# Performance work log

Measured on AMD Instinct MI355X. Metric: run time of the kernel, lower is better.

## Reference

```python
import jax, jax.numpy as jnp
import numpy as np

N, E, D = 50000, 500000, 128   # nodes, edges, input feature dim
H, F = 4, 32                    # num_heads, features_per_head (H*F == MLP output 128)


def _layer_norm(x, scale, bias, eps=1e-6):
    mu = jnp.mean(x, axis=-1, keepdims=True)
    var = jnp.var(x, axis=-1, keepdims=True)
    return (x - mu) * jax.lax.rsqrt(var + eps) * scale + bias


def setup_inputs() -> dict:
    key = jax.random.key(0)
    ks = jax.random.split(key, 6)
    s = lambda fan_in: 1.0 / np.sqrt(fan_in)
    return {
        "nodes": jax.random.normal(ks[0], (N, D), jnp.float32),
        "W1": jax.random.normal(ks[1], (D, 128), jnp.float32) * s(D),
        "b1": jnp.zeros((128,), jnp.float32),
        "ln1_scale": jnp.ones((128,), jnp.float32),
        "ln1_bias": jnp.zeros((128,), jnp.float32),
        "W2": jax.random.normal(ks[2], (128, H * F), jnp.float32) * s(128),
        "b2": jnp.zeros((H * F,), jnp.float32),
        "ln2_scale": jnp.ones((H * F,), jnp.float32),
        "ln2_bias": jnp.zeros((H * F,), jnp.float32),
        "senders": jax.random.randint(ks[3], (E,), 0, N, dtype=jnp.int32),
        "receivers": jax.random.randint(ks[4], (E,), 0, N, dtype=jnp.int32),
    }


def reference(nodes, W1, b1, ln1_scale, ln1_bias, W2, b2, ln2_scale, ln2_bias,
              senders, receivers):
    # attention_query MLP (MLPTorso: Dense -> LayerNorm -> relu, activate_final=True)
    h = jnp.maximum(_layer_norm(nodes @ W1 + b1, ln1_scale, ln1_bias), 0.0)
    h = jnp.maximum(_layer_norm(h @ W2 + b2, ln2_scale, ln2_bias), 0.0)
    q = h.reshape(N, H, F)                       # [N, H, F]

    # gather per-edge sender/receiver projections (same math as per-edge MLP)
    sent = q[senders]                            # [E, H, F]
    recv = q[receivers]                          # [E, H, F]

    # per-edge, per-head attention logits
    logits = jnp.einsum('ehf,ehf->eh', sent, recv) / jnp.sqrt(jnp.float32(F))

    # segment softmax over incoming edges of each receiver node (jraph semantics)
    seg_max = jax.ops.segment_max(logits, receivers, num_segments=N)
    seg_max = jnp.where(jnp.isfinite(seg_max), seg_max, 0.0)  # empty segments
    unnorm = jnp.exp(logits - seg_max[receivers])
    denom = jax.ops.segment_sum(unnorm, receivers, num_segments=N)
    weights = unnorm / denom[receivers]          # [E, H]

    # weighted messages, scatter-sum to receiver nodes
    messages = sent * weights[..., None]         # [E, H, F]
    agg = jax.ops.segment_sum(messages, receivers, num_segments=N)  # [N, H, F]

    # node update: activation then average over heads (avg_multi_head=True)
    out = jnp.maximum(agg, 0.0)
    return jnp.mean(out, axis=1)                 # [N, F]
```

## Files before the change

kernel.cpp:

```cpp
#include <hip/hip_runtime.h>

constexpr int D  = 128;
constexpr int NH = 4;
constexpr int NF = 32;

typedef __attribute__((ext_vector_type(8))) short bfrag;
typedef __attribute__((ext_vector_type(4))) float ffrag;

__device__ __forceinline__ unsigned short bf16h(float x) {
    unsigned u = __float_as_uint(x);
    u += 0x7fffu + ((u >> 16) & 1u);
    return (unsigned short)(u >> 16);
}
__device__ __forceinline__ float bf16tof(unsigned short h) {
    return __uint_as_float(((unsigned)h) << 16);
}

__global__ __launch_bounds__(256) void zero_cnt_kernel(int* __restrict__ p, int n)
{
    const int i4 = (blockIdx.x * blockDim.x + threadIdx.x) * 4;
    if (i4 + 3 < n) {
        *(int4*)&p[i4] = {0, 0, 0, 0};
    } else if (i4 < n) {
        for (int i = i4; i < n; ++i) p[i] = 0;
    }
}

__global__ __launch_bounds__(256) void wsplit_kernel(
    const float* __restrict__ W1, const float* __restrict__ W2,
    unsigned short* __restrict__ wt)
{
    __shared__ float T[32][33];
    const int L  = blockIdx.x >> 4;
    const int t  = blockIdx.x & 15;
    const int tr = t >> 2, tc = t & 3;
    const float* W = L ? W2 : W1;
    unsigned short* Hp = wt + (size_t)L * 32768;
    unsigned short* Lp = Hp + 16384;
    const int tx = threadIdx.x & 31, ty = threadIdx.x >> 5;
    #pragma unroll
    for (int i = 0; i < 4; ++i)
        T[ty + 8*i][tx] = W[(size_t)(tr*32 + ty + 8*i) * 128 + tc*32 + tx];
    __syncthreads();
    #pragma unroll
    for (int i = 0; i < 4; ++i) {
        const int c = tc*32 + ty + 8*i;
        const int k = tr*32 + tx;
        const float v = T[tx][ty + 8*i];
        const unsigned short hh = bf16h(v);
        const unsigned short ll = bf16h(v - bf16tof(hh));
        Hp[c*128 + k] = hh;
        Lp[c*128 + k] = ll;
    }
}

__global__ __launch_bounds__(256, 2) void mlp_mfma_kernel(
    const float* __restrict__ X,
    const unsigned short* __restrict__ WT,
    const float* __restrict__ b1, const float* __restrict__ g1, const float* __restrict__ be1,
    const float* __restrict__ b2, const float* __restrict__ g2, const float* __restrict__ be2,
    unsigned short* __restrict__ Q, int N)
{
    constexpr int P = 136;
    __shared__ unsigned short Xh[64 * P];
    __shared__ unsigned short Xl[64 * P];
    __shared__ unsigned short Wh[64 * P];
    __shared__ unsigned short Wl[64 * P];

    const int tid  = threadIdx.x;
    const int lane = tid & 63;
    const int wave = tid >> 6;
    const int n0   = blockIdx.x * 64;
    const int lc   = lane & 15;
    const int lg   = lane >> 4;

    #pragma unroll
    for (int j = 0; j < 8; ++j) {
        const int idx = tid + 256 * j;
        const int row = idx >> 5;
        const int c4  = (idx & 31) * 4;
        float4 v = {0, 0, 0, 0};
        if (n0 + row < N) v = *(const float4*)&X[(size_t)(n0 + row) * 128 + c4];
        const unsigned short h0 = bf16h(v.x), h1 = bf16h(v.y),
                             h2 = bf16h(v.z), h3 = bf16h(v.w);
        const unsigned short q0 = bf16h(v.x - bf16tof(h0)),
                             q1 = bf16h(v.y - bf16tof(h1)),
                             q2 = bf16h(v.z - bf16tof(h2)),
                             q3 = bf16h(v.w - bf16tof(h3));
        uint2 ph, pl;
        ph.x = (unsigned)h0 | ((unsigned)h1 << 16);
        ph.y = (unsigned)h2 | ((unsigned)h3 << 16);
        pl.x = (unsigned)q0 | ((unsigned)q1 << 16);
        pl.y = (unsigned)q2 | ((unsigned)q3 << 16);
        *(uint2*)&Xh[row * P + c4] = ph;
        *(uint2*)&Xl[row * P + c4] = pl;
    }

    auto stageW = [&](const unsigned short* Hg, const unsigned short* Lg, int half) {
        #pragma unroll
        for (int j = 0; j < 4; ++j) {
            const int u = tid + 256 * j;
            const int c = u >> 4;
            const int t = (u & 15) * 8;
            *(uint4*)&Wh[c * P + t] = *(const uint4*)&Hg[(size_t)(half*64 + c) * 128 + t];
            *(uint4*)&Wl[c * P + t] = *(const uint4*)&Lg[(size_t)(half*64 + c) * 128 + t];
        }
    };

    bfrag ah[4], al[4];
    auto loadA = [&]() {
        const int arow = wave * 16 + lc;
        #pragma unroll
        for (int ks = 0; ks < 4; ++ks) {
            ah[ks] = *(const bfrag*)&Xh[arow * P + ks * 32 + lg * 8];
            al[ks] = *(const bfrag*)&Xl[arow * P + ks * 32 + lg * 8];
        }
    };

    ffrag acc[8];
    auto gemmHalf = [&](int half) {
        #pragma unroll
        for (int ct = 0; ct < 4; ++ct) {
            const int crow = ct * 16 + lc;
            bfrag bh[4], bl[4];
            #pragma unroll
            for (int ks = 0; ks < 4; ++ks) {
                bh[ks] = *(const bfrag*)&Wh[crow * P + ks * 32 + lg * 8];
                bl[ks] = *(const bfrag*)&Wl[crow * P + ks * 32 + lg * 8];
            }
            ffrag a = acc[half * 4 + ct];
            #pragma unroll
            for (int ks = 0; ks < 4; ++ks) {
                a = __builtin_amdgcn_mfma_f32_16x16x32_bf16(ah[ks], bh[ks], a, 0, 0, 0);
                a = __builtin_amdgcn_mfma_f32_16x16x32_bf16(ah[ks], bl[ks], a, 0, 0, 0);
                a = __builtin_amdgcn_mfma_f32_16x16x32_bf16(al[ks], bh[ks], a, 0, 0, 0);
            }
            acc[half * 4 + ct] = a;
        }
    };

    const unsigned short* W1h = WT;
    const unsigned short* W1l = WT + 16384;
    const unsigned short* W2h = WT + 32768;
    const unsigned short* W2l = WT + 49152;

    #pragma unroll
    for (int i = 0; i < 8; ++i) acc[i] = (ffrag){0.f, 0.f, 0.f, 0.f};

    stageW(W1h, W1l, 0);
    __syncthreads();
    loadA();
    gemmHalf(0);
    __syncthreads();
    stageW(W1h, W1l, 1);
    __syncthreads();
    gemmHalf(1);

    {
        float bb[8], gg[8], tt[8];
        #pragma unroll
        for (int ct = 0; ct < 8; ++ct) {
            const int col = ct * 16 + lc;
            bb[ct] = b1[col]; gg[ct] = g1[col]; tt[ct] = be1[col];
        }
        #pragma unroll
        for (int j = 0; j < 4; ++j) {
            float t[8], s = 0.f, ss = 0.f;
            #pragma unroll
            for (int ct = 0; ct < 8; ++ct) {
                t[ct] = acc[ct][j] + bb[ct];
                s += t[ct]; ss += t[ct] * t[ct];
            }
            #pragma unroll
            for (int off = 1; off <= 8; off <<= 1) {
                s  += __shfl_xor(s,  off, 16);
                ss += __shfl_xor(ss, off, 16);
            }
            const float mu   = s * (1.f / 128.f);
            const float var  = fmaxf(ss * (1.f / 128.f) - mu * mu, 0.f);
            const float rstd = rsqrtf(var + 1e-6f);
            const int rl = wave * 16 + lg * 4 + j;
            #pragma unroll
            for (int ct = 0; ct < 8; ++ct) {
                const float o = fmaxf((t[ct] - mu) * rstd * gg[ct] + tt[ct], 0.f);
                const unsigned short hh = bf16h(o);
                const unsigned short ll = bf16h(o - bf16tof(hh));
                Xh[rl * P + ct * 16 + lc] = hh;
                Xl[rl * P + ct * 16 + lc] = ll;
            }
        }
    }

    #pragma unroll
    for (int i = 0; i < 8; ++i) acc[i] = (ffrag){0.f, 0.f, 0.f, 0.f};

    __syncthreads();
    stageW(W2h, W2l, 0);
    __syncthreads();
    loadA();
    gemmHalf(0);
    __syncthreads();
    stageW(W2h, W2l, 1);
    __syncthreads();
    gemmHalf(1);

    {
        float bb[8], gg[8], tt[8];
        #pragma unroll
        for (int ct = 0; ct < 8; ++ct) {
            const int col = ct * 16 + lc;
            bb[ct] = b2[col]; gg[ct] = g2[col]; tt[ct] = be2[col];
        }
        #pragma unroll
        for (int j = 0; j < 4; ++j) {
            float t[8], s = 0.f, ss = 0.f;
            #pragma unroll
            for (int ct = 0; ct < 8; ++ct) {
                t[ct] = acc[ct][j] + bb[ct];
                s += t[ct]; ss += t[ct] * t[ct];
            }
            #pragma unroll
            for (int off = 1; off <= 8; off <<= 1) {
                s  += __shfl_xor(s,  off, 16);
                ss += __shfl_xor(ss, off, 16);
            }
            const float mu   = s * (1.f / 128.f);
            const float var  = fmaxf(ss * (1.f / 128.f) - mu * mu, 0.f);
            const float rstd = rsqrtf(var + 1e-6f);
            const int grow = n0 + wave * 16 + lg * 4 + j;
            if (grow < N) {
                #pragma unroll
                for (int ct = 0; ct < 8; ++ct) {
                    const float o = fmaxf((t[ct] - mu) * rstd * gg[ct] + tt[ct], 0.f);
                    Q[(size_t)grow * 128 + ct * 16 + lc] = bf16h(o);
                }
            }
        }
    }
}

__global__ __launch_bounds__(256) void hist_kernel(
    const int* __restrict__ recv, int* __restrict__ cnt, int E)
{
    int i = blockIdx.x * blockDim.x + threadIdx.x;
    if (i < E) atomicAdd(&cnt[recv[i]], 1);
}

__global__ __launch_bounds__(256) void scan_blocks_kernel(
    const int* __restrict__ cnt, int* __restrict__ rowptr,
    int* __restrict__ bsum, int N)
{
    __shared__ int lds[256];
    const int tid = threadIdx.x;
    const int base = blockIdx.x * 1024 + tid * 4;
    int v0 = (base + 0 < N) ? cnt[base + 0] : 0;
    int v1 = (base + 1 < N) ? cnt[base + 1] : 0;
    int v2 = (base + 2 < N) ? cnt[base + 2] : 0;
    int v3 = (base + 3 < N) ? cnt[base + 3] : 0;
    const int tsum = v0 + v1 + v2 + v3;
    lds[tid] = tsum;
    __syncthreads();
    for (int off = 1; off < 256; off <<= 1) {
        int t = (tid >= off) ? lds[tid - off] : 0;
        __syncthreads();
        lds[tid] += t;
        __syncthreads();
    }
    int run = lds[tid] - tsum;
    if (base + 0 < N) rowptr[base + 0] = run;
    run += v0;
    if (base + 1 < N) rowptr[base + 1] = run;
    run += v1;
    if (base + 2 < N) rowptr[base + 2] = run;
    run += v2;
    if (base + 3 < N) rowptr[base + 3] = run;
    if (tid == 255) bsum[blockIdx.x] = lds[255];
}

__global__ __launch_bounds__(256) void scan_top_kernel(int* bsum, int nb)
{
    __shared__ int lds[256];
    const int tid = threadIdx.x;
    int v = (tid < nb) ? bsum[tid] : 0;
    lds[tid] = v;
    __syncthreads();
    for (int off = 1; off < 256; off <<= 1) {
        int t = (tid >= off) ? lds[tid - off] : 0;
        __syncthreads();
        lds[tid] += t;
        __syncthreads();
    }
    if (tid < nb) bsum[tid] = lds[tid] - v;
}

__global__ __launch_bounds__(256) void scan_add_kernel(
    int* __restrict__ rowptr, int* __restrict__ cursor,
    const int* __restrict__ bsum, int N, int E)
{
    int i = blockIdx.x * blockDim.x + threadIdx.x;
    if (i < N) {
        int v = rowptr[i] + bsum[i >> 10];
        rowptr[i] = v;
        cursor[i] = v;
    }
    if (i == 0) rowptr[N] = E;
}

__global__ __launch_bounds__(256) void fill_kernel(
    const int* __restrict__ senders, const int* __restrict__ receivers,
    int* __restrict__ cursor, int* __restrict__ ssend, int E)
{
    int e = blockIdx.x * blockDim.x + threadIdx.x;
    if (e < E) {
        int r = receivers[e];
        int pos = atomicAdd(&cursor[r], 1);
        ssend[pos] = senders[e];
    }
}

__global__ __launch_bounds__(256) void node_attn_kernel(
    const unsigned short* __restrict__ q, const int* __restrict__ rowptr,
    const int* __restrict__ ssend, float* __restrict__ out, int N)
{
    const int lane = threadIdx.x & 63;
    const int hl   = lane & 31;
    const int half = lane >> 5;
    const int wid  = (blockIdx.x * blockDim.x + threadIdx.x) >> 6;
    const int nw   = (gridDim.x * blockDim.x) >> 6;

    for (int n = wid; n < N; n += nw) {
        const uint2 braw = *(const uint2*)&q[(size_t)n * D + hl * 4];
        const float b0 = __uint_as_float(braw.x << 16);
        const float b1 = __uint_as_float(braw.x & 0xffff0000u);
        const float b2 = __uint_as_float(braw.y << 16);
        const float b3 = __uint_as_float(braw.y & 0xffff0000u);

        const int beg = rowptr[n], end = rowptr[n + 1];
        float m = -1e30f, l = 0.f;
        float c0 = 0.f, c1 = 0.f, c2 = 0.f, c3 = 0.f;

        int j = beg + half;
        uint2 raw = {0u, 0u};
        if (j < end)
            raw = *(const uint2*)&q[(size_t)ssend[j] * D + hl * 4];
        for (; j < end; j += 2) {
            const uint2 cur = raw;
            if (j + 2 < end)
                raw = *(const uint2*)&q[(size_t)ssend[j + 2] * D + hl * 4];
            const float a0 = __uint_as_float(cur.x << 16);
            const float a1 = __uint_as_float(cur.x & 0xffff0000u);
            const float a2 = __uint_as_float(cur.y << 16);
            const float a3 = __uint_as_float(cur.y & 0xffff0000u);
            float p = a0 * b0 + a1 * b1 + a2 * b2 + a3 * b3;
            p += __shfl_xor(p, 1);
            p += __shfl_xor(p, 2);
            p += __shfl_xor(p, 4);
            const float logit = p * 0.17677669529663687f;
            const float nm = fmaxf(m, logit);
            const float sc = __expf(m - nm);
            const float u  = __expf(logit - nm);
            l  = l * sc + u;
            c0 = c0 * sc + u * a0;
            c1 = c1 * sc + u * a1;
            c2 = c2 * sc + u * a2;
            c3 = c3 * sc + u * a3;
            m = nm;
        }

        const float om  = __shfl_xor(m, 32);
        const float ol  = __shfl_xor(l, 32);
        const float oc0 = __shfl_xor(c0, 32);
        const float oc1 = __shfl_xor(c1, 32);
        const float oc2 = __shfl_xor(c2, 32);
        const float oc3 = __shfl_xor(c3, 32);
        const float nm = fmaxf(m, om);
        const float s0 = __expf(m - nm), s1 = __expf(om - nm);
        const float lt = l * s0 + ol * s1;
        const float inv = (lt > 0.f) ? (1.f / lt) : 0.f;
        float r0 = fmaxf((c0 * s0 + oc0 * s1) * inv, 0.f);
        float r1 = fmaxf((c1 * s0 + oc1 * s1) * inv, 0.f);
        float r2 = fmaxf((c2 * s0 + oc2 * s1) * inv, 0.f);
        float r3 = fmaxf((c3 * s0 + oc3 * s1) * inv, 0.f);

        r0 += __shfl_xor(r0, 8);  r0 += __shfl_xor(r0, 16);
        r1 += __shfl_xor(r1, 8);  r1 += __shfl_xor(r1, 16);
        r2 += __shfl_xor(r2, 8);  r2 += __shfl_xor(r2, 16);
        r3 += __shfl_xor(r3, 8);  r3 += __shfl_xor(r3, 16);
        if (lane < 8) {
            float4 o = {0.25f * r0, 0.25f * r1, 0.25f * r2, 0.25f * r3};
            *(float4*)&out[(size_t)n * NF + lane * 4] = o;
        }
    }
}

extern "C" void kernel_launch(void* const* d_in, const int* in_sizes, int n_in,
                              void* d_out, int out_size, void* d_ws, size_t ws_size,
                              hipStream_t stream)
{
    const float* nodes = (const float*)d_in[0];
    const float* W1    = (const float*)d_in[1];
    const float* b1    = (const float*)d_in[2];
    const float* g1    = (const float*)d_in[3];
    const float* be1   = (const float*)d_in[4];
    const float* W2    = (const float*)d_in[5];
    const float* b2    = (const float*)d_in[6];
    const float* g2    = (const float*)d_in[7];
    const float* be2   = (const float*)d_in[8];
    const int* senders   = (const int*)d_in[9];
    const int* receivers = (const int*)d_in[10];

    const int N = in_sizes[0] / D;
    const int E = in_sizes[9];
    float* out = (float*)d_out;

    char* ws = (char*)d_ws;
    unsigned short* qb = (unsigned short*)ws; ws += (size_t)N * D * 2;
    unsigned short* wt = (unsigned short*)ws; ws += 4 * 128 * 128 * 2;
    int* cnt      = (int*)ws;    ws += (size_t)N * 4;
    int* rowptr   = (int*)ws;    ws += (size_t)(N + 2) * 4;
    int* cursor   = (int*)ws;    ws += (size_t)N * 4;
    int* bsum     = (int*)ws;    ws += 256 * 4;
    int* ssend    = (int*)ws;    ws += (size_t)E * 4;

    zero_cnt_kernel<<<(N / 4 + 255) / 256, 256, 0, stream>>>(cnt, N);

    wsplit_kernel<<<32, 256, 0, stream>>>(W1, W2, wt);
    const int gblk = (N + 63) / 64;
    mlp_mfma_kernel<<<gblk, 256, 0, stream>>>(nodes, wt, b1, g1, be1,
                                              b2, g2, be2, qb, N);

    const int nb = (N + 1023) / 1024;
    hist_kernel<<<(E + 255) / 256, 256, 0, stream>>>(receivers, cnt, E);
    scan_blocks_kernel<<<nb, 256, 0, stream>>>(cnt, rowptr, bsum, N);
    scan_top_kernel<<<1, 256, 0, stream>>>(bsum, nb);
    scan_add_kernel<<<(N + 255) / 256, 256, 0, stream>>>(rowptr, cursor, bsum, N, E);
    fill_kernel<<<(E + 255) / 256, 256, 0, stream>>>(senders, receivers, cursor, ssend, E);

    node_attn_kernel<<<(N + 3) / 4, 256, 0, stream>>>(qb, rowptr, ssend, out, N);
}
```

Measured before the change: 134.4 us.

## Pre-swizzle weights into MFMA fragment order and drop shared-memory staging in MLP

The weight-split kernel now writes W1/W2 hi/lo bf16 parts directly in per-lane MFMA fragment order. The MLP kernel then loads B fragments straight from global memory (L2-resident) instead of staging them through shared memory with block barriers. Each wave processes its own 16 rows independently, converting X in registers and round-tripping the hidden layer through a small per-wave LDS buffer. This removes __syncthreads and cuts LDS use so the launch bound can rise to 4 blocks per CU, at the cost of repeated global/L2 weight fetches per wave.

```diff
diff --git a/kernel.cpp b/kernel.cpp
--- a/kernel.cpp
+++ b/kernel.cpp
@@ -30,131 +30,89 @@
     const float* __restrict__ W1, const float* __restrict__ W2,
     unsigned short* __restrict__ wt)
 {
-    __shared__ float T[32][33];
-    const int L  = blockIdx.x >> 4;
-    const int t  = blockIdx.x & 15;
-    const int tr = t >> 2, tc = t & 3;
+    const int L  = blockIdx.x >> 3;
+    const int ct = blockIdx.x & 7;
     const float* W = L ? W2 : W1;
-    unsigned short* Hp = wt + (size_t)L * 32768;
-    unsigned short* Lp = Hp + 16384;
-    const int tx = threadIdx.x & 31, ty = threadIdx.x >> 5;
+    const int ks   = threadIdx.x >> 6;
+    const int lane = threadIdx.x & 63;
+    const int lg = lane >> 4, lc = lane & 15;
+    unsigned short* Hp = wt + ((size_t)(L * 2 + 0) * 32 + ct * 4 + ks) * 512 + lane * 8;
+    unsigned short* Lp = wt + ((size_t)(L * 2 + 1) * 32 + ct * 4 + ks) * 512 + lane * 8;
     #pragma unroll
-    for (int i = 0; i < 4; ++i)
-        T[ty + 8*i][tx] = W[(size_t)(tr*32 + ty + 8*i) * 128 + tc*32 + tx];
-    __syncthreads();
-    #pragma unroll
-    for (int i = 0; i < 4; ++i) {
-        const int c = tc*32 + ty + 8*i;
-        const int k = tr*32 + tx;
-        const float v = T[tx][ty + 8*i];
+    for (int i = 0; i < 8; ++i) {
+        const int k = ks * 32 + lg * 8 + i;
+        const int c = ct * 16 + lc;
+        const float v = W[(size_t)k * 128 + c];
         const unsigned short hh = bf16h(v);
-        const unsigned short ll = bf16h(v - bf16tof(hh));
-        Hp[c*128 + k] = hh;
-        Lp[c*128 + k] = ll;
-    }
-}
-
-__global__ __launch_bounds__(256, 2) void mlp_mfma_kernel(
+        Hp[i] = hh;
+        Lp[i] = bf16h(v - bf16tof(hh));
+    }
+}
+
+__global__ __launch_bounds__(256, 4) void mlp_mfma_kernel(
     const float* __restrict__ X,
-    const unsigned short* __restrict__ WT,
+    const unsigned short* __restrict__ WF,
     const float* __restrict__ b1, const float* __restrict__ g1, const float* __restrict__ be1,
     const float* __restrict__ b2, const float* __restrict__ g2, const float* __restrict__ be2,
     unsigned short* __restrict__ Q, int N)
 {
-    constexpr int P = 136;
-    __shared__ unsigned short Xh[64 * P];
-    __shared__ unsigned short Xl[64 * P];
-    __shared__ unsigned short Wh[64 * P];
-    __shared__ unsigned short Wl[64 * P];
+    constexpr int PW = 132;
+    __shared__ unsigned HL[4 * 16 * PW];
 
     const int tid  = threadIdx.x;
     const int lane = tid & 63;
     const int wave = tid >> 6;
-    const int n0   = blockIdx.x * 64;
     const int lc   = lane & 15;
     const int lg   = lane >> 4;
-
-    #pragma unroll
-    for (int j = 0; j < 8; ++j) {
-        const int idx = tid + 256 * j;
-        const int row = idx >> 5;
-        const int c4  = (idx & 31) * 4;
-        float4 v = {0, 0, 0, 0};
-        if (n0 + row < N) v = *(const float4*)&X[(size_t)(n0 + row) * 128 + c4];
-        const unsigned short h0 = bf16h(v.x), h1 = bf16h(v.y),
-                             h2 = bf16h(v.z), h3 = bf16h(v.w);
-        const unsigned short q0 = bf16h(v.x - bf16tof(h0)),
-                             q1 = bf16h(v.y - bf16tof(h1)),
-                             q2 = bf16h(v.z - bf16tof(h2)),
-                             q3 = bf16h(v.w - bf16tof(h3));
-        uint2 ph, pl;
-        ph.x = (unsigned)h0 | ((unsigned)h1 << 16);
-        ph.y = (unsigned)h2 | ((unsigned)h3 << 16);
-        pl.x = (unsigned)q0 | ((unsigned)q1 << 16);
-        pl.y = (unsigned)q2 | ((unsigned)q3 << 16);
-        *(uint2*)&Xh[row * P + c4] = ph;
-        *(uint2*)&Xl[row * P + c4] = pl;
-    }
-
-    auto stageW = [&](const unsigned short* Hg, const unsigned short* Lg, int half) {
-        #pragma unroll
-        for (int j = 0; j < 4; ++j) {
-            const int u = tid + 256 * j;
-            const int c = u >> 4;
-            const int t = (u & 15) * 8;
-            *(uint4*)&Wh[c * P + t] = *(const uint4*)&Hg[(size_t)(half*64 + c) * 128 + t];
-            *(uint4*)&Wl[c * P + t] = *(const uint4*)&Lg[(size_t)(half*64 + c) * 128 + t];
-        }
-    };
+    const int n0w  = (blockIdx.x * 4 + wave) * 16;
+    if (n0w >= N) return;
+    unsigned* hl = &HL[wave * 16 * PW];
 
     bfrag ah[4], al[4];
-    auto loadA = [&]() {
-        const int arow = wave * 16 + lc;
+    ffrag acc[8];
+
+    {
+        const int rowx = (n0w + lc < N) ? (n0w + lc) : (N - 1);
+        const float* xr = X + (size_t)rowx * 128 + lg * 8;
         #pragma unroll
         for (int ks = 0; ks < 4; ++ks) {
-            ah[ks] = *(const bfrag*)&Xh[arow * P + ks * 32 + lg * 8];
-            al[ks] = *(const bfrag*)&Xl[arow * P + ks * 32 + lg * 8];
-        }
-    };
-
-    ffrag acc[8];
-    auto gemmHalf = [&](int half) {
-        #pragma unroll
-        for (int ct = 0; ct < 4; ++ct) {
-            const int crow = ct * 16 + lc;
+            const float4 a = *(const float4*)&xr[ks * 32];
+            const float4 b = *(const float4*)&xr[ks * 32 + 4];
+            const float f[8] = {a.x, a.y, a.z, a.w, b.x, b.y, b.z, b.w};
+            #pragma unroll
+            for (int i = 0; i < 8; ++i) {
+                const unsigned short hh = bf16h(f[i]);
+                ah[ks][i] = (short)hh;
+                al[ks][i] = (short)bf16h(f[i] - bf16tof(hh));
+            }
+        }
+    }
+
+    auto gemm = [&](int hiBase, int loBase) {
+        #pragma unroll
+        for (int ct = 0; ct < 8; ++ct) {
+            const unsigned short* bhp = WF + (size_t)(hiBase + ct * 4) * 512 + lane * 8;
+            const unsigned short* blp = WF + (size_t)(loBase + ct * 4) * 512 + lane * 8;
             bfrag bh[4], bl[4];
             #pragma unroll
             for (int ks = 0; ks < 4; ++ks) {
-                bh[ks] = *(const bfrag*)&Wh[crow * P + ks * 32 + lg * 8];
-                bl[ks] = *(const bfrag*)&Wl[crow * P + ks * 32 + lg * 8];
-            }
-            ffrag a = acc[half * 4 + ct];
+                bh[ks] = *(const bfrag*)(bhp + ks * 512);
+                bl[ks] = *(const bfrag*)(blp + ks * 512);
+            }
+            ffrag a = acc[ct];
             #pragma unroll
             for (int ks = 0; ks < 4; ++ks) {
                 a = __builtin_amdgcn_mfma_f32_16x16x32_bf16(ah[ks], bh[ks], a, 0, 0, 0);
                 a = __builtin_amdgcn_mfma_f32_16x16x32_bf16(ah[ks], bl[ks], a, 0, 0, 0);
                 a = __builtin_amdgcn_mfma_f32_16x16x32_bf16(al[ks], bh[ks], a, 0, 0, 0);
             }
-            acc[half * 4 + ct] = a;
+            acc[ct] = a;
         }
     };
-
-    const unsigned short* W1h = WT;
-    const unsigned short* W1l = WT + 16384;
-    const unsigned short* W2h = WT + 32768;
-    const unsigned short* W2l = WT + 49152;
 
     #pragma unroll
     for (int i = 0; i < 8; ++i) acc[i] = (ffrag){0.f, 0.f, 0.f, 0.f};
-
-    stageW(W1h, W1l, 0);
-    __syncthreads();
-    loadA();
-    gemmHalf(0);
-    __syncthreads();
-    stageW(W1h, W1l, 1);
-    __syncthreads();
-    gemmHalf(1);
+    gemm(0, 32);
 
     {
         float bb[8], gg[8], tt[8];
@@ -179,30 +137,34 @@
             const float mu   = s * (1.f / 128.f);
             const float var  = fmaxf(ss * (1.f / 128.f) - mu * mu, 0.f);
             const float rstd = rsqrtf(var + 1e-6f);
-            const int rl = wave * 16 + lg * 4 + j;
+            const int row = lg * 4 + j;
             #pragma unroll
             for (int ct = 0; ct < 8; ++ct) {
                 const float o = fmaxf((t[ct] - mu) * rstd * gg[ct] + tt[ct], 0.f);
                 const unsigned short hh = bf16h(o);
                 const unsigned short ll = bf16h(o - bf16tof(hh));
-                Xh[rl * P + ct * 16 + lc] = hh;
-                Xl[rl * P + ct * 16 + lc] = ll;
-            }
+                hl[row * PW + ct * 16 + lc] = (unsigned)hh | ((unsigned)ll << 16);
+            }
+        }
+    }
+
+    asm volatile("s_waitcnt lgkmcnt(0)" ::: "memory");
+
+    #pragma unroll
+    for (int ks = 0; ks < 4; ++ks) {
+        const uint4 r0 = *(const uint4*)&hl[lc * PW + ks * 32 + lg * 8];
+        const uint4 r1 = *(const uint4*)&hl[lc * PW + ks * 32 + lg * 8 + 4];
+        const unsigned rr[8] = {r0.x, r0.y, r0.z, r0.w, r1.x, r1.y, r1.z, r1.w};
+        #pragma unroll
+        for (int i = 0; i < 8; ++i) {
+            ah[ks][i] = (short)(rr[i] & 0xffffu);
+            al[ks][i] = (short)(rr[i] >> 16);
         }
     }
 
     #pragma unroll
     for (int i = 0; i < 8; ++i) acc[i] = (ffrag){0.f, 0.f, 0.f, 0.f};
-
-    __syncthreads();
-    stageW(W2h, W2l, 0);
-    __syncthreads();
-    loadA();
-    gemmHalf(0);
-    __syncthreads();
-    stageW(W2h, W2l, 1);
-    __syncthreads();
-    gemmHalf(1);
+    gemm(64, 96);
 
     {
         float bb[8], gg[8], tt[8];
@@ -227,7 +189,7 @@
             const float mu   = s * (1.f / 128.f);
             const float var  = fmaxf(ss * (1.f / 128.f) - mu * mu, 0.f);
             const float rstd = rsqrtf(var + 1e-6f);
-            const int grow = n0 + wave * 16 + lg * 4 + j;
+            const int grow = n0w + lg * 4 + j;
             if (grow < N) {
                 #pragma unroll
                 for (int ct = 0; ct < 8; ++ct) {
@@ -424,8 +386,9 @@
 
     zero_cnt_kernel<<<(N / 4 + 255) / 256, 256, 0, stream>>>(cnt, N);
 
-    wsplit_kernel<<<32, 256, 0, stream>>>(W1, W2, wt);
-    const int gblk = (N + 63) / 64;
+    wsplit_kernel<<<16, 256, 0, stream>>>(W1, W2, wt);
+    const int nwaves = (N + 15) / 16;
+    const int gblk = (nwaves + 3) / 4;
     mlp_mfma_kernel<<<gblk, 256, 0, stream>>>(nodes, wt, b1, g1, be1,
                                               b2, g2, be2, qb, N);
 
```

After: 132.9 us. About the same (-1.2%).
